# Performance work log

Measured on AMD Instinct MI355X. Metric: run time of the kernel, lower is better.

## Reference

```python
import jax, jax.numpy as jnp
import numpy as np

N = 8192        # points
M = 131072      # query-key pairs (edges)
C_IN = 512
H = 8           # heads
D = 64          # head_channels
BINS = 48
BIN_SIZE = 0.05


def setup_inputs() -> dict:
    key = jax.random.key(0)
    ks = jax.random.split(key, 8)
    x_F = jax.random.normal(ks[0], (N, C_IN), dtype=jnp.float32)
    x_C = jax.random.uniform(ks[1], (N, 3), dtype=jnp.float32)
    qk_pair_idxs = jax.random.randint(ks[2], (2, M), 0, N, dtype=jnp.int64)
    W_qkv = jax.random.normal(ks[3], (C_IN, 3 * H * D), dtype=jnp.float32) * 0.02
    b_qkv = jnp.zeros((3 * H * D,), dtype=jnp.float32)
    q_tables = jax.random.normal(ks[4], (3, BINS, H, D), dtype=jnp.float32) * 0.02
    k_tables = jax.random.normal(ks[5], (3, BINS, H, D), dtype=jnp.float32) * 0.02
    v_tables = jax.random.normal(ks[6], (3, BINS, H, D), dtype=jnp.float32) * 0.02
    return {"x_F": x_F, "x_C": x_C, "qk_pair_idxs": qk_pair_idxs,
            "W_qkv": W_qkv, "b_qkv": b_qkv,
            "q_tables": q_tables, "k_tables": k_tables, "v_tables": v_tables}


def reference(x_F, x_C, qk_pair_idxs, W_qkv, b_qkv, q_tables, k_tables, v_tables):
    n = x_F.shape[0]
    qkv = (x_F @ W_qkv + b_qkv).reshape(n, 3, H, D)
    q = qkv[:, 0] * (D ** -0.5)   # scale folded into queries, as in the module
    k = qkv[:, 1]
    v = qkv[:, 2]
    qi = qk_pair_idxs[0]
    ki = qk_pair_idxs[1]
    # quantized relative coordinates -> table bin indices [M,3]
    rel = (x_C[qi] - x_C[ki]) / BIN_SIZE + BINS / 2
    idx = jnp.clip(rel.astype(jnp.int32), 0, BINS - 1)
    # precompute per-point, per-axis, per-bin table dot products [N,3,BINS,H]
    q_dot = jnp.einsum('nhd,abhd->nabh', q, q_tables)
    k_dot = jnp.einsum('nhd,abhd->nabh', k, k_tables)
    # content logits [M,H]
    logits = jnp.einsum('mhd,mhd->mh', q[qi], k[ki])
    for a in range(3):  # fixed xyz axes
        logits = logits + q_dot[qi, a, idx[:, a]] + k_dot[ki, a, idx[:, a]]
    # scatter softmax over query index (per head)
    seg_max = jax.ops.segment_max(logits, qi, num_segments=n)
    e = jnp.exp(logits - seg_max[qi])
    denom = jax.ops.segment_sum(e, qi, num_segments=n)
    attn = e / denom[qi]  # [M,H]
    # value-side relative position bias, summed over axes [M,H,D]
    vt = v_tables[0, idx[:, 0]] + v_tables[1, idx[:, 1]] + v_tables[2, idx[:, 2]]
    contrib = attn[:, :, None] * (v[ki] + vt)            # [M,H,D]
    agg = jax.ops.segment_sum(contrib, qi, num_segments=n)  # [N,H,D]
    return agg.reshape(n, H * D)
```

## Files before the change

kernel.cpp:

```cpp
#include <hip/hip_runtime.h>
#include <hip/hip_bf16.h>
#include <stdint.h>

#define N_PTS 8192
#define M_EDGES 131072
#define CIN 512
#define QKV_COLS 1536

typedef __bf16 bf16x8 __attribute__((ext_vector_type(8)));
typedef float f32x4 __attribute__((ext_vector_type(4)));

#define GAS __attribute__((address_space(1)))
#define LAS __attribute__((address_space(3)))

__device__ __forceinline__ void gload_lds16(const void* g, void* l) {
  __builtin_amdgcn_global_load_lds((const GAS void*)g, (LAS void*)l, 16, 0, 0);
}

__global__ __launch_bounds__(256) void prep_kernel(
    const float* __restrict__ xF, const float* __restrict__ W,
    const float* __restrict__ qt, const float* __restrict__ kt,
    const float* __restrict__ vt, const int* __restrict__ pairs,
    const float* __restrict__ xc,
    __bf16* __restrict__ A, __bf16* __restrict__ BT,
    __bf16* __restrict__ qtb, __bf16* __restrict__ ktb, __bf16* __restrict__ vtT,
    int* __restrict__ qi_a, unsigned* __restrict__ pack0, int* __restrict__ cnt) {
  __shared__ float tile[32][33];
  int b = blockIdx.x;
  int tid = threadIdx.x;
  if (b < 4096) {
    int base = (b * 256 + tid) * 4;
    float4 v = *(const float4*)(xF + base);
    A[base + 0] = (__bf16)v.x;
    A[base + 1] = (__bf16)v.y;
    A[base + 2] = (__bf16)v.z;
    A[base + 3] = (__bf16)v.w;
  } else if (b < 4864) {
    int blk = b - 4096;
    int bk = blk & 15, bn = blk >> 4;
    int x = tid & 31, y = tid >> 5;
#pragma unroll
    for (int j = 0; j < 4; j++) {
      int r = y + j * 8;
      tile[r][x] = W[(size_t)(bk * 32 + r) * QKV_COLS + bn * 32 + x];
    }
    __syncthreads();
#pragma unroll
    for (int j = 0; j < 4; j++) {
      int r = y + j * 8;
      BT[(size_t)(bn * 32 + r) * CIN + bk * 32 + x] = (__bf16)tile[x][r];
    }
  } else if (b < 5152) {
    int i = (b - 4864) * 256 + tid;
    int d = i & 63, h = (i >> 6) & 7, ab = i >> 9;
    int po = (h * 144 + ab) * 64 + d;
    qtb[po] = (__bf16)qt[i];
    ktb[po] = (__bf16)kt[i];
  } else if (b < 5472) {
    int i = (b - 5152) * 256 + tid;
    int p = i % 160;
    int d = (i / 160) & 63;
    int h = i / 10240;
    vtT[i] = (p < 144) ? (__bf16)vt[p * 512 + h * 64 + d] : (__bf16)0.f;
  } else {
    int m = (b - 5472) * 256 + tid;
    int qi = pairs[m], ki = pairs[M_EDGES + m];
    unsigned pb = 0;
#pragma unroll
    for (int a = 0; a < 3; a++) {
      float rel = (xc[qi * 3 + a] - xc[ki * 3 + a]) / 0.05f + 24.0f;
      int bb = (int)rel;
      bb = bb < 0 ? 0 : (bb > 47 ? 47 : bb);
      pb |= (unsigned)bb << (6 * a);
    }
    qi_a[m] = qi;
    pack0[m] = (unsigned)ki | (pb << 13);
    atomicAdd(&cnt[qi], 1);
  }
}

__global__ __launch_bounds__(256) void gemm_qkv(const __bf16* __restrict__ A,
                                                const __bf16* __restrict__ BT,
                                                const float* __restrict__ bias,
                                                __bf16* __restrict__ qb,
                                                __bf16* __restrict__ kb,
                                                __bf16* __restrict__ vb) {
  __shared__ __align__(16) char At[2][64 * 128];
  __shared__ __align__(16) char Bt[2][128 * 128];
  int tid = threadIdx.x;
  int w = tid >> 6, l = tid & 63;
  int bn = blockIdx.x, bm = blockIdx.y;
  int wm = w & 1, wn = w >> 1;
  f32x4 acc[2][4] = {};
  const char* Ab = (const char*)A;
  const char* Bb = (const char*)BT;
  int lr = l & 15;
  int lk = (l >> 4) * 16;
  int xr = (lr & 7) << 4;

  auto stage = [&](int tk, int buf) {
#pragma unroll
    for (int r = 0; r < 2; r++) {
      int flat = r * 4096 + tid * 16;
      int row = flat >> 7, colb = flat & 127;
      int gcolb = colb ^ ((row & 7) << 4);
      gload_lds16(Ab + ((size_t)(bm * 64 + row) * CIN + tk * 64) * 2 + gcolb,
                  At[buf] + r * 4096 + w * 1024);
    }
#pragma unroll
    for (int r = 0; r < 4; r++) {
      int flat = r * 4096 + tid * 16;
      int row = flat >> 7, colb = flat & 127;
      int gcolb = colb ^ ((row & 7) << 4);
      gload_lds16(Bb + ((size_t)(bn * 128 + row) * CIN + tk * 64) * 2 + gcolb,
                  Bt[buf] + r * 4096 + w * 1024);
    }
  };

  stage(0, 0);
  __syncthreads();
  int cur = 0;
  for (int kt = 0; kt < 8; kt++) {
    if (kt < 7) stage(kt + 1, cur ^ 1);
#pragma unroll
    for (int ks = 0; ks < 2; ks++) {
      bf16x8 af[2], bfr[4];
      int cs = (ks * 64 + lk) ^ xr;
#pragma unroll
      for (int mf = 0; mf < 2; mf++) af[mf] = *(const bf16x8*)(At[cur] + (wm * 32 + mf * 16 + lr) * 128 + cs);
#pragma unroll
      for (int nf = 0; nf < 4; nf++) bfr[nf] = *(const bf16x8*)(Bt[cur] + (wn * 64 + nf * 16 + lr) * 128 + cs);
#pragma unroll
      for (int mf = 0; mf < 2; mf++)
#pragma unroll
        for (int nf = 0; nf < 4; nf++)
          acc[mf][nf] = __builtin_amdgcn_mfma_f32_16x16x32_bf16(af[mf], bfr[nf], acc[mf][nf], 0, 0, 0);
    }
    __syncthreads();
    cur ^= 1;
  }

  int lg = l >> 4;
#pragma unroll
  for (int mf = 0; mf < 2; mf++) {
#pragma unroll
    for (int nf = 0; nf < 4; nf++) {
      int gc = bn * 128 + wn * 64 + nf * 16 + lr;
      float b = bias[gc];
      int which = gc >> 9;
      int col = gc & 511;
      __bf16* dst = which == 0 ? qb : (which == 1 ? kb : vb);
      float scale = which == 0 ? 0.125f : 1.0f;
#pragma unroll
      for (int j = 0; j < 4; j++) {
        int gr = bm * 64 + wm * 32 + mf * 16 + lg * 4 + j;
        dst[(size_t)gr * 512 + col] = (__bf16)((acc[mf][nf][j] + b) * scale);
      }
    }
  }
}

__global__ __launch_bounds__(256) void table_dot(const __bf16* __restrict__ qb,
                                                 const __bf16* __restrict__ kb,
                                                 const __bf16* __restrict__ qtb,
                                                 const __bf16* __restrict__ ktb,
                                                 __bf16* __restrict__ qdot,
                                                 __bf16* __restrict__ kdot) {
  __shared__ __align__(16) char As[128 * 128];
  __shared__ __align__(16) char Bs[144 * 128];
  int nt = blockIdx.x, h = blockIdx.y, z = blockIdx.z;
  const __bf16* src = z ? kb : qb;
  const __bf16* tab = z ? ktb : qtb;
  __bf16* out = z ? kdot : qdot;
  int tid = threadIdx.x, w = tid >> 6, l = tid & 63;
  const char* sb = (const char*)src;
  const char* tb = (const char*)tab + (size_t)h * 144 * 128;
#pragma unroll
  for (int p = 0; p < 4; p++) {
    int flat = p * 4096 + tid * 16;
    int row = flat >> 7, colb = flat & 127;
    int gcolb = colb ^ ((row & 7) << 4);
    gload_lds16(sb + (size_t)(nt * 128 + row) * 1024 + h * 128 + gcolb, As + p * 4096 + w * 1024);
    gload_lds16(tb + row * 128 + gcolb, Bs + p * 4096 + w * 1024);
  }
  if (w < 2) {
    int flat = 16384 + w * 1024 + l * 16;
    int row = flat >> 7, colb = flat & 127;
    int gcolb = colb ^ ((row & 7) << 4);
    gload_lds16(tb + row * 128 + gcolb, Bs + 16384 + w * 1024);
  }
  __syncthreads();

  f32x4 acc[2][9] = {};
  int lr = l & 15, lk = (l >> 4) * 16;
  int xr = (lr & 7) << 4;
#pragma unroll
  for (int ks = 0; ks < 2; ks++) {
    bf16x8 af[2], bf[9];
    int cs = (ks * 64 + lk) ^ xr;
#pragma unroll
    for (int mf = 0; mf < 2; mf++)
      af[mf] = *(const bf16x8*)(As + (w * 32 + mf * 16 + lr) * 128 + cs);
#pragma unroll
    for (int nf = 0; nf < 9; nf++)
      bf[nf] = *(const bf16x8*)(Bs + (nf * 16 + lr) * 128 + cs);
#pragma unroll
    for (int mf = 0; mf < 2; mf++)
#pragma unroll
      for (int nf = 0; nf < 9; nf++)
        acc[mf][nf] = __builtin_amdgcn_mfma_f32_16x16x32_bf16(af[mf], bf[nf], acc[mf][nf], 0, 0, 0);
  }

  int lg = l >> 4;
#pragma unroll
  for (int mf = 0; mf < 2; mf++)
#pragma unroll
    for (int nf = 0; nf < 9; nf++)
#pragma unroll
      for (int j = 0; j < 4; j++) {
        int n = nt * 128 + w * 32 + mf * 16 + lg * 4 + j;
        int ab = nf * 16 + lr;
        out[(size_t)n * 1152 + ab * 8 + h] = (__bf16)acc[mf][nf][j];
      }
}

__global__ __launch_bounds__(256) void scan_kernel(const int* __restrict__ cnt,
                                                   int* __restrict__ off,
                                                   int* __restrict__ cursor) {
  __shared__ int wsum[4];
  int tid = threadIdx.x, lane = tid & 63, w = tid >> 6;
  int local[32];
  int s = 0;
#pragma unroll
  for (int i = 0; i < 8; i++) {
    int4 v = ((const int4*)cnt)[tid * 8 + i];
    local[i * 4 + 0] = v.x; local[i * 4 + 1] = v.y;
    local[i * 4 + 2] = v.z; local[i * 4 + 3] = v.w;
    s += v.x + v.y + v.z + v.w;
  }
  int incl = s;
#pragma unroll
  for (int d = 1; d < 64; d <<= 1) {
    int t = __shfl_up(incl, d, 64);
    if (lane >= d) incl += t;
  }
  if (lane == 63) wsum[w] = incl;
  __syncthreads();
  int woff = 0;
#pragma unroll
  for (int j = 0; j < 4; j++) woff += (j < w) ? wsum[j] : 0;
  int run = woff + incl - s;
  int base = tid * 32;
#pragma unroll
  for (int i = 0; i < 32; i++) {
    off[base + i] = run;
    cursor[base + i] = run;
    run += local[i];
  }
  if (tid == 255) off[N_PTS] = run;
}

__global__ void scatter_k(const int* __restrict__ qi_a, const unsigned* __restrict__ pack0,
                          int* __restrict__ cursor, unsigned* __restrict__ epack) {
  int m = blockIdx.x * blockDim.x + threadIdx.x;
  if (m < M_EDGES) {
    int qi = qi_a[m];
    int pos = atomicAdd(&cursor[qi], 1);
    epack[pos] = pack0[m];
  }
}

__global__ __launch_bounds__(512) void attn_kernel(
    const __bf16* __restrict__ qb, const __bf16* __restrict__ kb,
    const __bf16* __restrict__ vb, const __bf16* __restrict__ qdot,
    const __bf16* __restrict__ kdot, const int* __restrict__ off,
    const unsigned* __restrict__ epack,
    float* __restrict__ num, float* __restrict__ den, __bf16* __restrict__ Hb) {
  __shared__ float hist[8 * 160];
  int n = blockIdx.x;
  int tid = threadIdx.x;
  int h = tid >> 6, l = tid & 63;
  int es = l >> 3, dg = l & 7;
  int tcol = h * 64 + dg * 8;

  for (int i = tid; i < 1280; i += 512) hist[i] = 0.f;
  __syncthreads();

  bf16x8 q8 = *(const bf16x8*)(qb + (n << 9) + tcol);
  float qv[8];
#pragma unroll
  for (int j = 0; j < 8; j++) qv[j] = (float)q8[j];

  float acc[8] = {0.f, 0.f, 0.f, 0.f, 0.f, 0.f, 0.f, 0.f};
  float dn = 0.f;
  int e0 = off[n], e1 = off[n + 1];
  const __bf16* qd_row = qdot + (size_t)n * 1152;
  int axis = dg < 3 ? dg : dg - 3;
  int tsh = 6 * axis;

  for (int base = e0; base < e1; base += 8) {
    int e = base + es;
    bool valid = e < e1;
    int ee = valid ? e : e0;
    unsigned pk = epack[ee];
    int ki = pk & 8191;
    unsigned pb = pk >> 13;
    bf16x8 k8 = *(const bf16x8*)(kb + (ki << 9) + tcol);
    bf16x8 v8 = *(const bf16x8*)(vb + (ki << 9) + tcol);
    int bin = (int)((pb >> tsh) & 63u);
    int idx = (axis * 48 + bin) * 8 + h;
    const __bf16* tbl = dg < 3 ? qd_row : (kdot + (size_t)ki * 1152);
    float p = (dg < 6) ? (float)tbl[idx] : 0.f;
#pragma unroll
    for (int j = 0; j < 8; j++) p += qv[j] * (float)k8[j];
    p += __shfl_xor(p, 1, 64);
    p += __shfl_xor(p, 2, 64);
    p += __shfl_xor(p, 4, 64);
    float x = valid ? __expf(p) : 0.f;
    dn += x;
#pragma unroll
    for (int j = 0; j < 8; j++) acc[j] += x * (float)v8[j];
    if (dg == 0 && valid) {
      float* hh = hist + h * 160;
      atomicAdd(hh + (pb & 63), x);
      atomicAdd(hh + 48 + ((pb >> 6) & 63), x);
      atomicAdd(hh + 96 + ((pb >> 12) & 63), x);
    }
  }

#pragma unroll
  for (int s = 8; s <= 32; s <<= 1) {
    dn += __shfl_xor(dn, s, 64);
#pragma unroll
    for (int j = 0; j < 8; j++) acc[j] += __shfl_xor(acc[j], s, 64);
  }

  if (l < 8) {
    float* op = num + (n << 9) + h * 64 + l * 8;
    f32x4 o0 = {acc[0], acc[1], acc[2], acc[3]};
    f32x4 o1 = {acc[4], acc[5], acc[6], acc[7]};
    *(f32x4*)op = o0;
    *(f32x4*)(op + 4) = o1;
  }
  if (l == 0) den[n * 8 + h] = dn;
  __syncthreads();
  for (int i = tid; i < 1280; i += 512) Hb[(size_t)n * 1280 + i] = (__bf16)hist[i];
}

__global__ __launch_bounds__(256) void finish_kernel(const __bf16* __restrict__ Hb,
                                                     const __bf16* __restrict__ vtT,
                                                     const float* __restrict__ den,
                                                     float* __restrict__ out) {
  __shared__ __align__(16) char As[2][128 * 64];
  __shared__ __align__(16) char Bs[2][64 * 64];
  int nt = blockIdx.x, h = blockIdx.y;
  int tid = threadIdx.x, w = tid >> 6, l = tid & 63;
  int lr = l & 15, lk = (l >> 4) * 16;
  int xr = (lr & 3) << 4;
  const char* Ab = (const char*)Hb;
  const char* Bb = (const char*)vtT;
  f32x4 acc[2][4] = {};

  auto stage = [&](int tk, int buf) {
#pragma unroll
    for (int c = 0; c < 2; c++) {
      int flat = c * 4096 + tid * 16;
      int row = flat >> 6, colb = flat & 63;
      int gcolb = colb ^ ((row & 3) << 4);
      gload_lds16(Ab + ((size_t)(nt * 128 + row) * 1280 + h * 160 + tk * 32) * 2 + gcolb,
                  As[buf] + c * 4096 + w * 1024);
    }
    {
      int flat = tid * 16;
      int row = flat >> 6, colb = flat & 63;
      int gcolb = colb ^ ((row & 3) << 4);
      gload_lds16(Bb + ((size_t)(h * 64 + row) * 160 + tk * 32) * 2 + gcolb,
                  Bs[buf] + w * 1024);
    }
  };

  stage(0, 0);
  __syncthreads();
  int cur = 0;
  for (int kt = 0; kt < 5; kt++) {
    if (kt < 4) stage(kt + 1, cur ^ 1);
    bf16x8 af[2], bf[4];
    int cs = lk ^ xr;
#pragma unroll
    for (int mf = 0; mf < 2; mf++) af[mf] = *(const bf16x8*)(As[cur] + (w * 32 + mf * 16 + lr) * 64 + cs);
#pragma unroll
    for (int nf = 0; nf < 4; nf++) bf[nf] = *(const bf16x8*)(Bs[cur] + (nf * 16 + lr) * 64 + cs);
#pragma unroll
    for (int mf = 0; mf < 2; mf++)
#pragma unroll
      for (int nf = 0; nf < 4; nf++)
        acc[mf][nf] = __builtin_amdgcn_mfma_f32_16x16x32_bf16(af[mf], bf[nf], acc[mf][nf], 0, 0, 0);
    __syncthreads();
    cur ^= 1;
  }

  int lg = l >> 4;
#pragma unroll
  for (int mf = 0; mf < 2; mf++) {
#pragma unroll
    for (int j = 0; j < 4; j++) {
      int n = nt * 128 + w * 32 + mf * 16 + lg * 4 + j;
      float dnv = den[n * 8 + h];
      float inv = dnv > 0.f ? 1.f / dnv : 0.f;
#pragma unroll
      for (int nf = 0; nf < 4; nf++) {
        int gi = (n << 9) + h * 64 + nf * 16 + lr;
        out[gi] = (out[gi] + acc[mf][nf][j]) * inv;
      }
    }
  }
}

extern "C" void kernel_launch(void* const* d_in, const int* in_sizes, int n_in,
                              void* d_out, int out_size, void* d_ws, size_t ws_size,
                              hipStream_t stream) {
  const float* xF = (const float*)d_in[0];
  const float* xC = (const float*)d_in[1];
  const int* pairs = (const int*)d_in[2];
  const float* W = (const float*)d_in[3];
  const float* bias = (const float*)d_in[4];
  const float* qt = (const float*)d_in[5];
  const float* kt = (const float*)d_in[6];
  const float* vt = (const float*)d_in[7];
  float* out = (float*)d_out;

  char* ws = (char*)d_ws;
  size_t o = 0;
  auto alloc = [&](size_t bytes) {
    void* p = ws + o;
    o = (o + bytes + 255) & ~(size_t)255;
    return p;
  };
  char* region0 = (char*)alloc((size_t)N_PTS * 1280 * 2);
  __bf16* A = (__bf16*)region0;
  __bf16* BT = (__bf16*)(region0 + (size_t)N_PTS * CIN * 2);
  __bf16* Hb = (__bf16*)region0;
  __bf16* qb = (__bf16*)alloc((size_t)N_PTS * 512 * 2);
  __bf16* kb = (__bf16*)alloc((size_t)N_PTS * 512 * 2);
  __bf16* vb = (__bf16*)alloc((size_t)N_PTS * 512 * 2);
  __bf16* qtb = (__bf16*)alloc((size_t)8 * 144 * 64 * 2);
  __bf16* ktb = (__bf16*)alloc((size_t)8 * 144 * 64 * 2);
  __bf16* vtT = (__bf16*)alloc((size_t)8 * 64 * 160 * 2);
  __bf16* qdot = (__bf16*)alloc((size_t)N_PTS * 1152 * 2);
  __bf16* kdot = (__bf16*)alloc((size_t)N_PTS * 1152 * 2);
  float* den = (float*)alloc((size_t)N_PTS * 8 * 4);
  int* qi_a = (int*)alloc(M_EDGES * 4);
  unsigned* pack0 = (unsigned*)alloc(M_EDGES * 4);
  unsigned* epack = (unsigned*)alloc(M_EDGES * 4);
  int* cnt = (int*)alloc(N_PTS * 4);
  int* off = (int*)alloc((N_PTS + 1) * 4);
  int* cursor = (int*)alloc(N_PTS * 4);

  hipMemsetAsync(cnt, 0, N_PTS * 4, stream);

  prep_kernel<<<5984, 256, 0, stream>>>(xF, W, qt, kt, vt, pairs, xC,
                                        A, BT, qtb, ktb, vtT, qi_a, pack0, cnt);
  scan_kernel<<<1, 256, 0, stream>>>(cnt, off, cursor);
  scatter_k<<<M_EDGES / 256, 256, 0, stream>>>(qi_a, pack0, cursor, epack);
  gemm_qkv<<<dim3(QKV_COLS / 128, N_PTS / 64), 256, 0, stream>>>(A, BT, bias, qb, kb, vb);
  table_dot<<<dim3(N_PTS / 128, 8, 2), 256, 0, stream>>>(qb, kb, qtb, ktb, qdot, kdot);
  attn_kernel<<<N_PTS, 512, 0, stream>>>(qb, kb, vb, qdot, kdot, off, epack, out, den, Hb);
  finish_kernel<<<dim3(N_PTS / 128, 8), 256, 0, stream>>>(Hb, vtT, den, out);
}
```

Baseline: 164.9 us.

## Assign one edge per wavefront across all heads in attention kernel

Changes the attention kernel's work split so each wavefront processes a whole edge across all 8 heads, with lanes covering the 512 channels, instead of each wave handling one head over 8 edges. Edge indices become wave-uniform via readfirstlane, which removes the validity masking and lets K/V rows be read as contiguous 1 KB loads. Per-wave partial sums are now combined through shared memory instead of cross-lane shuffles. The histogram rows are padded to 164 floats to reduce LDS bank conflicts on the atomics. This costs 16 KB of extra shared memory per block, and low-degree points leave some waves idle.

```diff
diff --git a/kernel.cpp b/kernel.cpp
--- a/kernel.cpp
+++ b/kernel.cpp
@@ -276,17 +276,18 @@
     const __bf16* __restrict__ kdot, const int* __restrict__ off,
     const unsigned* __restrict__ epack,
     float* __restrict__ num, float* __restrict__ den, __bf16* __restrict__ Hb) {
-  __shared__ float hist[8 * 160];
+  __shared__ float hist[8 * 164];
+  __shared__ float part[8][512];
+  __shared__ float dpart[8][8];
   int n = blockIdx.x;
   int tid = threadIdx.x;
-  int h = tid >> 6, l = tid & 63;
-  int es = l >> 3, dg = l & 7;
-  int tcol = h * 64 + dg * 8;
-
-  for (int i = tid; i < 1280; i += 512) hist[i] = 0.f;
-  __syncthreads();
-
-  bf16x8 q8 = *(const bf16x8*)(qb + (n << 9) + tcol);
+  int w = tid >> 6, l = tid & 63;
+  int h = l >> 3, dg = l & 7;
+
+  for (int i = tid; i < 8 * 164; i += 512) hist[i] = 0.f;
+  __syncthreads();
+
+  bf16x8 q8 = *(const bf16x8*)(qb + (n << 9) + l * 8);
   float qv[8];
 #pragma unroll
   for (int j = 0; j < 8; j++) qv[j] = (float)q8[j];
@@ -298,15 +299,12 @@
   int axis = dg < 3 ? dg : dg - 3;
   int tsh = 6 * axis;
 
-  for (int base = e0; base < e1; base += 8) {
-    int e = base + es;
-    bool valid = e < e1;
-    int ee = valid ? e : e0;
-    unsigned pk = epack[ee];
+  for (int e = e0 + w; e < e1; e += 8) {
+    unsigned pk = epack[__builtin_amdgcn_readfirstlane(e)];
     int ki = pk & 8191;
     unsigned pb = pk >> 13;
-    bf16x8 k8 = *(const bf16x8*)(kb + (ki << 9) + tcol);
-    bf16x8 v8 = *(const bf16x8*)(vb + (ki << 9) + tcol);
+    bf16x8 k8 = *(const bf16x8*)(kb + (ki << 9) + l * 8);
+    bf16x8 v8 = *(const bf16x8*)(vb + (ki << 9) + l * 8);
     int bin = (int)((pb >> tsh) & 63u);
     int idx = (axis * 48 + bin) * 8 + h;
     const __bf16* tbl = dg < 3 ? qd_row : (kdot + (size_t)ki * 1152);
@@ -316,35 +314,39 @@
     p += __shfl_xor(p, 1, 64);
     p += __shfl_xor(p, 2, 64);
     p += __shfl_xor(p, 4, 64);
-    float x = valid ? __expf(p) : 0.f;
+    float x = __expf(p);
     dn += x;
 #pragma unroll
     for (int j = 0; j < 8; j++) acc[j] += x * (float)v8[j];
-    if (dg == 0 && valid) {
-      float* hh = hist + h * 160;
+    if (dg == 0) {
+      float* hh = hist + h * 164;
       atomicAdd(hh + (pb & 63), x);
       atomicAdd(hh + 48 + ((pb >> 6) & 63), x);
       atomicAdd(hh + 96 + ((pb >> 12) & 63), x);
     }
   }
 
-#pragma unroll
-  for (int s = 8; s <= 32; s <<= 1) {
-    dn += __shfl_xor(dn, s, 64);
-#pragma unroll
-    for (int j = 0; j < 8; j++) acc[j] += __shfl_xor(acc[j], s, 64);
-  }
-
-  if (l < 8) {
-    float* op = num + (n << 9) + h * 64 + l * 8;
-    f32x4 o0 = {acc[0], acc[1], acc[2], acc[3]};
-    f32x4 o1 = {acc[4], acc[5], acc[6], acc[7]};
-    *(f32x4*)op = o0;
-    *(f32x4*)(op + 4) = o1;
-  }
-  if (l == 0) den[n * 8 + h] = dn;
-  __syncthreads();
-  for (int i = tid; i < 1280; i += 512) Hb[(size_t)n * 1280 + i] = (__bf16)hist[i];
+  f32x4 a0 = {acc[0], acc[1], acc[2], acc[3]};
+  f32x4 a1 = {acc[4], acc[5], acc[6], acc[7]};
+  *(f32x4*)&part[w][l * 8] = a0;
+  *(f32x4*)&part[w][l * 8 + 4] = a1;
+  if (dg == 0) dpart[w][h] = dn;
+  __syncthreads();
+
+  float s = 0.f;
+#pragma unroll
+  for (int ww = 0; ww < 8; ww++) s += part[ww][tid];
+  num[(n << 9) + tid] = s;
+  if (tid < 8) {
+    float d = 0.f;
+#pragma unroll
+    for (int ww = 0; ww < 8; ww++) d += dpart[ww][tid];
+    den[n * 8 + tid] = d;
+  }
+  for (int i = tid; i < 1280; i += 512) {
+    int hh = i / 160, p = i % 160;
+    Hb[(size_t)n * 1280 + i] = (__bf16)hist[hh * 164 + p];
+  }
 }
 
 __global__ __launch_bounds__(256) void finish_kernel(const __bf16* __restrict__ Hb,
```

Measured after the change: 156.8 us. -4.9%, faster.
